# Performance work log

Measured on AMD Instinct MI355X. Metric: run time of the kernel, lower is better.

The kernel has to match this reference:

```python
import jax, jax.numpy as jnp
import numpy as np

N, E, D, A = 50000, 1_600_000, 32, 2
H1, C1, H2, C2 = 4, 16, 2, 32  # GATv2Conv(D,16,heads=4) -> 64; GATv2Conv(64,32,heads=2) -> 64


def setup_inputs() -> dict:
    key = jax.random.key(0)
    ks = jax.random.split(key, 16)

    def glorot(k, shape):
        fan = shape[0] + shape[-1]
        return jax.random.normal(k, shape, jnp.float32) * np.float32(np.sqrt(2.0 / fan))

    return {
        "x": jax.random.normal(ks[0], (N, D), jnp.float32),
        "edge_index": jax.random.randint(ks[1], (2, E), 0, N),
        "edge_attr": jax.random.normal(ks[2], (E, 2), jnp.float32),
        # GATv2 layer 1 (lin_l/lin_r with bias, lin_edge no bias, att [H,C], out bias)
        "w1_l": glorot(ks[3], (D, H1 * C1)), "b1_l": jnp.zeros((H1 * C1,), jnp.float32),
        "w1_r": glorot(ks[4], (D, H1 * C1)), "b1_r": jnp.zeros((H1 * C1,), jnp.float32),
        "w1_e": glorot(ks[5], (2, H1 * C1)),
        "att1": glorot(ks[6], (H1, C1)),
        "bias1": jnp.zeros((H1 * C1,), jnp.float32),
        # GATv2 layer 2
        "w2_l": glorot(ks[7], (H1 * C1, H2 * C2)), "b2_l": jnp.zeros((H2 * C2,), jnp.float32),
        "w2_r": glorot(ks[8], (H1 * C1, H2 * C2)), "b2_r": jnp.zeros((H2 * C2,), jnp.float32),
        "w2_e": glorot(ks[9], (2, H2 * C2)),
        "att2": glorot(ks[10], (H2, C2)),
        "bias2": jnp.zeros((H2 * C2,), jnp.float32),
        # heads
        "w_actor": glorot(ks[11], (H2 * C2, A)), "b_actor": jnp.zeros((A,), jnp.float32),
        "w_critic": glorot(ks[12], (H2 * C2, 1)), "b_critic": jnp.zeros((1,), jnp.float32),
        "log_std": jnp.zeros((A,), jnp.float32),
    }


def _gatv2(x, src, dst, eattr, Wl, bl, Wr, br, We, att, bias, H, C, n):
    # PyG GATv2Conv: message j->i with i = dst, j = src
    xl = (x @ Wl + bl).reshape(n, H, C)  # source-side transform (x_j)
    xr = (x @ Wr + br).reshape(n, H, C)  # target-side transform (x_i)
    ee = (eattr @ We).reshape(-1, H, C)  # per-edge embedding
    z = jax.nn.leaky_relu(xl[src] + xr[dst] + ee, 0.2)  # [Etot, H, C]
    logits = jnp.einsum('ehc,hc->eh', z, att)  # [Etot, H]
    # segment softmax over incoming edges of each dst node
    m = jax.ops.segment_max(logits, dst, num_segments=n)
    p = jnp.exp(logits - m[dst])
    denom = jax.ops.segment_sum(p, dst, num_segments=n)
    alpha = p / denom[dst]  # every node has a self-loop -> denom > 0
    msg = xl[src] * alpha[:, :, None]  # [Etot, H, C]
    out = jax.ops.segment_sum(msg, dst, num_segments=n)
    return out.reshape(n, H * C) + bias


def reference(x, edge_index, edge_attr,
              w1_l, b1_l, w1_r, b1_r, w1_e, att1, bias1,
              w2_l, b2_l, w2_r, b2_r, w2_e, att2, bias2,
              w_actor, b_actor, w_critic, b_critic, log_std):
    src, dst = edge_index[0], edge_index[1]
    # add_self_loops=True, fill_value='mean': self-loop edge_attr = mean of incoming edge_attr
    cnt = jax.ops.segment_sum(jnp.ones((edge_attr.shape[0],), x.dtype), dst, num_segments=N)
    sums = jax.ops.segment_sum(edge_attr, dst, num_segments=N)
    loop_attr = sums / jnp.maximum(cnt, 1.0)[:, None]
    loop = jnp.arange(N, dtype=src.dtype)
    src_f = jnp.concatenate([src, loop])
    dst_f = jnp.concatenate([dst, loop])
    ea = jnp.concatenate([edge_attr, loop_attr], axis=0)

    h = jax.nn.relu(_gatv2(x, src_f, dst_f, ea, w1_l, b1_l, w1_r, b1_r, w1_e, att1, bias1, H1, C1, N))
    h = jax.nn.relu(_gatv2(h, src_f, dst_f, ea, w2_l, b2_l, w2_r, b2_r, w2_e, att2, bias2, H2, C2, N))

    action_mean = jnp.tanh(h @ w_actor + b_actor)  # [N, A]
    value = h @ w_critic + b_critic               # [N, 1]
    std = jnp.exp(log_std)                        # [A]  (Normal(action_mean, std))
    return action_mean, std, value
```

## Files before the change

kernel.cpp:

```cpp
#include <hip/hip_runtime.h>
#include <math.h>

#define DIN   32
#define F1    64
#define F2    64

template <int K>
__device__ __forceinline__ void lin_lr_body(int bid,
        const float* __restrict__ x,
        const float* __restrict__ Wl, const float* __restrict__ bl,
        const float* __restrict__ Wr, const float* __restrict__ br,
        float* __restrict__ xl, float* __restrict__ xr, int n) {
    __shared__ float Ash[32][K + 4];
    __shared__ float Wsh[K][128];
    const int t = threadIdx.x;
    const int node0 = bid * 32;

    for (int idx = t; idx < 32 * (K / 4); idx += 256) {
        int m = idx / (K / 4), kq = idx % (K / 4);
        float4 v = make_float4(0.f, 0.f, 0.f, 0.f);
        if (node0 + m < n) v = ((const float4*)(x + (size_t)(node0 + m) * K))[kq];
        *(float4*)&Ash[m][kq * 4] = v;
    }
    for (int idx = t; idx < K * 32; idx += 256) {
        int k = idx / 32, j4 = idx % 32;
        float4 v = (j4 < 16) ? ((const float4*)(Wl + (size_t)k * 64))[j4]
                             : ((const float4*)(Wr + (size_t)k * 64))[j4 - 16];
        *(float4*)&Wsh[k][j4 * 4] = v;
    }
    __syncthreads();

    const int ty = t >> 4;
    const int tx = t & 15;
    float acc0[8], acc1[8];
#pragma unroll
    for (int j = 0; j < 8; j++) { acc0[j] = 0.f; acc1[j] = 0.f; }

#pragma unroll 4
    for (int k = 0; k < K; k++) {
        float a0 = Ash[ty * 2 + 0][k];
        float a1 = Ash[ty * 2 + 1][k];
        float4 w0 = *(const float4*)&Wsh[k][tx * 8];
        float4 w1 = *(const float4*)&Wsh[k][tx * 8 + 4];
        acc0[0] += a0 * w0.x; acc0[1] += a0 * w0.y;
        acc0[2] += a0 * w0.z; acc0[3] += a0 * w0.w;
        acc0[4] += a0 * w1.x; acc0[5] += a0 * w1.y;
        acc0[6] += a0 * w1.z; acc0[7] += a0 * w1.w;
        acc1[0] += a1 * w0.x; acc1[1] += a1 * w0.y;
        acc1[2] += a1 * w0.z; acc1[3] += a1 * w0.w;
        acc1[4] += a1 * w1.x; acc1[5] += a1 * w1.y;
        acc1[6] += a1 * w1.z; acc1[7] += a1 * w1.w;
    }

    const float* bsrc = (tx < 8) ? bl : br;
    int jb = (tx < 8) ? tx * 8 : (tx - 8) * 8;
    float4 b0 = ((const float4*)(bsrc + jb))[0];
    float4 b1 = ((const float4*)(bsrc + jb))[1];
    float* dst = (tx < 8) ? xl : xr;
#pragma unroll
    for (int m = 0; m < 2; m++) {
        int node = node0 + ty * 2 + m;
        if (node >= n) continue;
        const float* ac = (m == 0) ? acc0 : acc1;
        float4 o0, o1;
        o0.x = ac[0] + b0.x; o0.y = ac[1] + b0.y;
        o0.z = ac[2] + b0.z; o0.w = ac[3] + b0.w;
        o1.x = ac[4] + b1.x; o1.y = ac[5] + b1.y;
        o1.z = ac[6] + b1.z; o1.w = ac[7] + b1.w;
        ((float4*)(dst + (size_t)node * 64 + jb))[0] = o0;
        ((float4*)(dst + (size_t)node * 64 + jb))[1] = o1;
    }
}

__global__ __launch_bounds__(256, 2)
void fused_bcount_lin1(const int* __restrict__ dstr, int* __restrict__ cnt_mat,
                       int E, int Ec, int NB, int gridLin,
                       const float* __restrict__ x,
                       const float* __restrict__ Wl, const float* __restrict__ bl,
                       const float* __restrict__ Wr, const float* __restrict__ br,
                       float* __restrict__ xl, float* __restrict__ xr, int n) {
    __shared__ int hist[256];
    if ((int)blockIdx.x < gridLin) {
        lin_lr_body<DIN>(blockIdx.x, x, Wl, bl, Wr, br, xl, xr, n);
        return;
    }
    const int blk = blockIdx.x - gridLin;
    const int t = threadIdx.x;
    hist[t] = 0;
    __syncthreads();
    const int s0 = blk * Ec, s1 = min(E, s0 + Ec);
    for (int e = s0 + t; e < s1; e += 256)
        atomicAdd(&hist[dstr[e] >> 8], 1);
    __syncthreads();
    if (t < NB) cnt_mat[t * 256 + blk] = hist[t];
}


__global__ void scan_blocks(const int* __restrict__ cnt, int* __restrict__ partial,
                            int* __restrict__ btot, int n) {
    __shared__ int sh[256];
    int t = threadIdx.x;
    int i = blockIdx.x * 256 + t;
    int v = (i < n) ? cnt[i] : 0;
    sh[t] = v; __syncthreads();
    for (int off = 1; off < 256; off <<= 1) {
        int x = (t >= off) ? sh[t - off] : 0;
        __syncthreads();
        sh[t] += x;
        __syncthreads();
    }
    if (i < n) partial[i] = sh[t] - v;
    if (t == 255) btot[blockIdx.x] = sh[t];
}

__global__ void scan_top(int* __restrict__ btot, int nb) {
    __shared__ int sh[256];
    int t = threadIdx.x;
    int v = (t < nb) ? btot[t] : 0;
    sh[t] = v; __syncthreads();
    for (int off = 1; off < 256; off <<= 1) {
        int x = (t >= off) ? sh[t - off] : 0;
        __syncthreads();
        sh[t] += x;
        __syncthreads();
    }
    if (t < nb) btot[t] = sh[t] - v;
}

__global__ void scan_add(const int* __restrict__ partial, const int* __restrict__ boff,
                         int* __restrict__ out, int n) {
    int i = blockIdx.x * blockDim.x + threadIdx.x;
    if (i >= n) return;
    out[i] = partial[i] + boff[i >> 8];
}

__global__ __launch_bounds__(256)
void scatter_buckets(const int* __restrict__ srcr, const int* __restrict__ dstr,
                     const float* __restrict__ ea, const int* __restrict__ colbase,
                     int4* __restrict__ inter, int E, int Ec) {
    __shared__ int hist[256];
    const int blk = blockIdx.x;
    const int t = threadIdx.x;
    hist[t] = 0;
    __syncthreads();
    const int s0 = blk * Ec, s1 = min(E, s0 + Ec);
    for (int e = s0 + t; e < s1; e += 256) {
        int d = dstr[e];
        int b = d >> 8;
        int lr = atomicAdd(&hist[b], 1);
        float2 v = ((const float2*)ea)[e];
        int4 r;
        r.x = srcr[e];
        r.y = __float_as_int(v.x);
        r.z = __float_as_int(v.y);
        r.w = d;
        inter[colbase[b * 256 + blk] + lr] = r;
    }
}

__global__ __launch_bounds__(256)
void bucket_csr(const int4* __restrict__ inter, const int* __restrict__ colbase,
                int* __restrict__ row_ptr, int4* __restrict__ edges,
                int NB, int N, int E) {
    __shared__ int sh[256];
    __shared__ int lscan[256];
    __shared__ int cur[256];
    const int b = blockIdx.x, t = threadIdx.x;
    const int bstart = colbase[b * 256];
    const int bend = (b + 1 < NB) ? colbase[(b + 1) * 256] : E;

    sh[t] = 0;
    __syncthreads();
    for (int pos = bstart + t; pos < bend; pos += 256)
        atomicAdd(&sh[inter[pos].w & 255], 1);
    __syncthreads();
    int v = sh[t];
    __syncthreads();
    sh[t] = v; __syncthreads();
    for (int off = 1; off < 256; off <<= 1) {
        int x = (t >= off) ? sh[t - off] : 0;
        __syncthreads();
        sh[t] += x;
        __syncthreads();
    }
    int excl = sh[t] - v;
    lscan[t] = excl;
    cur[t] = excl;
    int node = b * 256 + t;
    if (node <= N) row_ptr[node] = bstart + excl;
    __syncthreads();
    for (int pos = bstart + t; pos < bend; pos += 256) {
        int4 r = inter[pos];
        int k = atomicAdd(&cur[r.w & 255], 1);
        edges[bstart + k] = r;
    }
}

__global__ __launch_bounds__(256, 2)
void lin_lr_tiled64(const float* __restrict__ x,
                    const float* __restrict__ Wl, const float* __restrict__ bl,
                    const float* __restrict__ Wr, const float* __restrict__ br,
                    float* __restrict__ xl, float* __restrict__ xr, int n) {
    lin_lr_body<F1>(blockIdx.x, x, Wl, bl, Wr, br, xl, xr, n);
}

template <int H, int C>
__global__ __launch_bounds__(256)
void gat_kernel(const float* __restrict__ xl, const float* __restrict__ xr,
                const int* __restrict__ row_ptr, const int4* __restrict__ edges,
                const float* __restrict__ We, const float* __restrict__ att,
                const float* __restrict__ bias, float* __restrict__ out,
                int n, int E) {
    constexpr int LPH = C / 4;
    const int lane = threadIdx.x & 63;
    const int wid = (blockIdx.x * blockDim.x + threadIdx.x) >> 6;
    if (wid >= n) return;
    const int i = wid;
    const int g = lane >> 4;
    const int q = lane & 15;

    const float4 xri = ((const float4*)(xr + (size_t)i * 64))[q];
    const float4 we0 = ((const float4*)We)[q];
    const float4 we1 = ((const float4*)(We + 64))[q];
    float4 av = ((const float4*)att)[q];
    const float LOG2E = 1.4426950408889634f;
    av.x *= LOG2E; av.y *= LOG2E; av.z *= LOG2E; av.w *= LOG2E;

    float mx = -1e30f, den = 0.f;
    float a0 = 0.f, a1 = 0.f, a2 = 0.f, a3 = 0.f;
    float s0 = 0.f, s1 = 0.f;

    const int e0 = row_ptr[i], e1 = row_ptr[i + 1];

    int4 rn = edges[min(e0 + g, E - 1)];
    float4 xvn = ((const float4*)(xl + (size_t)rn.x * 64))[q];

    for (int eb = e0; eb < e1; eb += 4) {
        const bool valid = (eb + g) < e1;
        int4 r = rn;
        float4 xv = xvn;
        int idx = min(eb + 4 + g, E - 1);
        rn = edges[idx];
        xvn = ((const float4*)(xl + (size_t)rn.x * 64))[q];

        float ea0 = __int_as_float(r.y), ea1 = __int_as_float(r.z);
        if (!valid) { ea0 = 0.f; ea1 = 0.f; }
        s0 += ea0; s1 += ea1;
        float z0 = xv.x + fmaf(ea0, we0.x, ea1 * we1.x) + xri.x;
        float z1 = xv.y + fmaf(ea0, we0.y, ea1 * we1.y) + xri.y;
        float z2 = xv.z + fmaf(ea0, we0.z, ea1 * we1.z) + xri.z;
        float z3 = xv.w + fmaf(ea0, we0.w, ea1 * we1.w) + xri.w;
        z0 = (z0 > 0.f) ? z0 : 0.2f * z0;
        z1 = (z1 > 0.f) ? z1 : 0.2f * z1;
        z2 = (z2 > 0.f) ? z2 : 0.2f * z2;
        z3 = (z3 > 0.f) ? z3 : 0.2f * z3;
        float l = fmaf(z0, av.x, fmaf(z1, av.y, fmaf(z2, av.z, z3 * av.w)));
#pragma unroll
        for (int m = 1; m < LPH; m <<= 1) l += __shfl_xor(l, m, 64);
        if (!valid) l = -1e30f;
        float nm = fmaxf(mx, l);
        float sc = exp2f(mx - nm);
        float p  = exp2f(l - nm);
        den = den * sc + p;
        a0 = fmaf(a0, sc, p * xv.x);
        a1 = fmaf(a1, sc, p * xv.y);
        a2 = fmaf(a2, sc, p * xv.z);
        a3 = fmaf(a3, sc, p * xv.w);
        mx = nm;
    }

#pragma unroll
    for (int m = 16; m < 64; m <<= 1) {
        float omx  = __shfl_xor(mx, m, 64);
        float oden = __shfl_xor(den, m, 64);
        float o0 = __shfl_xor(a0, m, 64);
        float o1 = __shfl_xor(a1, m, 64);
        float o2 = __shfl_xor(a2, m, 64);
        float o3 = __shfl_xor(a3, m, 64);
        s0 += __shfl_xor(s0, m, 64);
        s1 += __shfl_xor(s1, m, 64);
        float nm = fmaxf(mx, omx);
        float sa = exp2f(mx - nm);
        float sb = exp2f(omx - nm);
        den = den * sa + oden * sb;
        a0 = fmaf(a0, sa, o0 * sb);
        a1 = fmaf(a1, sa, o1 * sb);
        a2 = fmaf(a2, sa, o2 * sb);
        a3 = fmaf(a3, sa, o3 * sb);
        mx = nm;
    }

    float degc = fmaxf((float)(e1 - e0), 1.0f);
    float la0 = s0 / degc, la1 = s1 / degc;
    const float4 xlv = ((const float4*)(xl + (size_t)i * 64))[q];
    {
        float z0 = xlv.x + fmaf(la0, we0.x, la1 * we1.x) + xri.x;
        float z1 = xlv.y + fmaf(la0, we0.y, la1 * we1.y) + xri.y;
        float z2 = xlv.z + fmaf(la0, we0.z, la1 * we1.z) + xri.z;
        float z3 = xlv.w + fmaf(la0, we0.w, la1 * we1.w) + xri.w;
        z0 = (z0 > 0.f) ? z0 : 0.2f * z0;
        z1 = (z1 > 0.f) ? z1 : 0.2f * z1;
        z2 = (z2 > 0.f) ? z2 : 0.2f * z2;
        z3 = (z3 > 0.f) ? z3 : 0.2f * z3;
        float l = fmaf(z0, av.x, fmaf(z1, av.y, fmaf(z2, av.z, z3 * av.w)));
#pragma unroll
        for (int m = 1; m < LPH; m <<= 1) l += __shfl_xor(l, m, 64);
        float nm = fmaxf(mx, l);
        float sc = exp2f(mx - nm);
        float p  = exp2f(l - nm);
        den = den * sc + p;
        a0 = fmaf(a0, sc, p * xlv.x);
        a1 = fmaf(a1, sc, p * xlv.y);
        a2 = fmaf(a2, sc, p * xlv.z);
        a3 = fmaf(a3, sc, p * xlv.w);
    }

    if (g == 0) {
        float rd = 1.0f / den;
        const float4 bv = ((const float4*)bias)[q];
        float4 o;
        o.x = fmaxf(fmaf(a0, rd, bv.x), 0.f);
        o.y = fmaxf(fmaf(a1, rd, bv.y), 0.f);
        o.z = fmaxf(fmaf(a2, rd, bv.z), 0.f);
        o.w = fmaxf(fmaf(a3, rd, bv.w), 0.f);
        ((float4*)(out + (size_t)i * 64))[q] = o;
    }
}

__global__ void heads_kernel(const float* __restrict__ h, const float* __restrict__ wa,
                             const float* __restrict__ ba, const float* __restrict__ wc,
                             const float* __restrict__ bc, const float* __restrict__ ls,
                             float* __restrict__ out, int n) {
    if (blockIdx.x == 0 && threadIdx.x < 2)
        out[(size_t)n * 2 + threadIdx.x] = expf(ls[threadIdx.x]);
    int lane = threadIdx.x & 63;
    int wid = (blockIdx.x * blockDim.x + threadIdx.x) >> 6;
    if (wid >= n) return;
    float hv = h[wid * 64 + lane];
    float d0 = hv * wa[lane * 2 + 0];
    float d1 = hv * wa[lane * 2 + 1];
    float d2 = hv * wc[lane];
#pragma unroll
    for (int m = 1; m < 64; m <<= 1) {
        d0 += __shfl_xor(d0, m, 64);
        d1 += __shfl_xor(d1, m, 64);
        d2 += __shfl_xor(d2, m, 64);
    }
    if (lane == 0) {
        out[wid * 2 + 0] = tanhf(d0 + ba[0]);
        out[wid * 2 + 1] = tanhf(d1 + ba[1]);
        out[(size_t)n * 2 + 2 + wid] = d2 + bc[0];
    }
}


extern "C" void kernel_launch(void* const* d_in, const int* in_sizes, int n_in,
                              void* d_out, int out_size, void* d_ws, size_t ws_size,
                              hipStream_t stream) {
    const float* x    = (const float*)d_in[0];
    const int*   ei   = (const int*)  d_in[1];
    const float* ea   = (const float*)d_in[2];
    const float* w1l  = (const float*)d_in[3];
    const float* b1l  = (const float*)d_in[4];
    const float* w1r  = (const float*)d_in[5];
    const float* b1r  = (const float*)d_in[6];
    const float* w1e  = (const float*)d_in[7];
    const float* att1 = (const float*)d_in[8];
    const float* bias1= (const float*)d_in[9];
    const float* w2l  = (const float*)d_in[10];
    const float* b2l  = (const float*)d_in[11];
    const float* w2r  = (const float*)d_in[12];
    const float* b2r  = (const float*)d_in[13];
    const float* w2e  = (const float*)d_in[14];
    const float* att2 = (const float*)d_in[15];
    const float* bias2= (const float*)d_in[16];
    const float* wa   = (const float*)d_in[17];
    const float* ba   = (const float*)d_in[18];
    const float* wc   = (const float*)d_in[19];
    const float* bc   = (const float*)d_in[20];
    const float* ls   = (const float*)d_in[21];

    const int N = in_sizes[0] / DIN;
    const int E = in_sizes[2] / 2;
    const int* srcr = ei;
    const int* dstr = ei + E;

    const int NB = (N + 255) >> 8;
    const int Ec = (E + 255) / 256;
    const int n2 = NB * 256;

    char* p = (char*)d_ws;
    auto alloc = [&](size_t bytes) -> void* {
        void* r = (void*)p;
        p += (bytes + 255) & ~(size_t)255;
        return r;
    };
    int*   cnt_mat = (int*)  alloc((size_t)n2 * 4);
    int*   partial = (int*)  alloc((size_t)n2 * 4);
    int*   btot    = (int*)  alloc(256 * 4);
    int*   colbase = (int*)  alloc((size_t)n2 * 4);
    int*   row_ptr = (int*)  alloc((size_t)(N + 1) * 4);
    int4*  edges   = (int4*) alloc((size_t)E * 16);
    float* xl      = (float*)alloc((size_t)N * F1 * 4);
    float* xr      = (float*)alloc((size_t)N * F1 * 4);
    float* h1      = (float*)alloc((size_t)N * F1 * 4);
    float* h2      = (float*)alloc((size_t)N * F2 * 4);
    int4* inter = (int4*)h1;
    (void)ws_size; (void)n_in; (void)out_size;

    const int TB = 256;
    int nbScan = (n2 + TB - 1) / TB;
    int gridN2 = nbScan;
    int gridGemm = (N + 31) / 32;
    int gridWave = (N + 3) / 4;

    fused_bcount_lin1<<<gridGemm + 256, TB, 0, stream>>>(
        dstr, cnt_mat, E, Ec, NB, gridGemm, x, w1l, b1l, w1r, b1r, xl, xr, N);
    scan_blocks<<<gridN2, TB, 0, stream>>>(cnt_mat, partial, btot, n2);
    scan_top<<<1, TB, 0, stream>>>(btot, nbScan);
    scan_add<<<gridN2, TB, 0, stream>>>(partial, btot, colbase, n2);
    scatter_buckets<<<256, TB, 0, stream>>>(srcr, dstr, ea, colbase, inter, E, Ec);
    bucket_csr<<<NB, TB, 0, stream>>>(inter, colbase, row_ptr, edges, NB, N, E);

    gat_kernel<4, 16><<<gridWave, TB, 0, stream>>>(xl, xr, row_ptr, edges,
                                                   w1e, att1, bias1, h1, N, E);
    lin_lr_tiled64<<<gridGemm, TB, 0, stream>>>(h1, w2l, b2l, w2r, b2r, xl, xr, N);
    gat_kernel<2, 32><<<gridWave, TB, 0, stream>>>(xl, xr, row_ptr, edges,
                                                   w2e, att2, bias2, h2, N, E);
    heads_kernel<<<gridWave, TB, 0, stream>>>(h2, wa, ba, wc, bc, ls, (float*)d_out, N);
}
```

Measured before the change: 349.1 us.

## Drop online-softmax max, fuse heads into layer-2 GAT, merge scan passes

The GAT kernel no longer tracks a running maximum for the segment softmax. It accumulates exp2(logit) directly, which removes one exp and the rescale FMAs per edge and simplifies the cross-group reduction to plain sums. The actor/critic heads are fused into the second GAT kernel through a template flag, so the h2 round trip and one launch disappear. The scan_top and scan_add kernels are merged into one kernel that reduces the preceding block totals itself. Skipping max subtraction risks overflow if attention logits become large, which is safe only for moderately scaled weights like the test ones.

```diff
diff --git a/kernel.cpp b/kernel.cpp
--- a/kernel.cpp
+++ b/kernel.cpp
@@ -113,25 +113,18 @@
     if (t == 255) btot[blockIdx.x] = sh[t];
 }
 
-__global__ void scan_top(int* __restrict__ btot, int nb) {
+__global__ void scan_add2(const int* __restrict__ partial, const int* __restrict__ btot,
+                          int* __restrict__ out, int n) {
     __shared__ int sh[256];
-    int t = threadIdx.x;
-    int v = (t < nb) ? btot[t] : 0;
-    sh[t] = v; __syncthreads();
-    for (int off = 1; off < 256; off <<= 1) {
-        int x = (t >= off) ? sh[t - off] : 0;
+    const int t = threadIdx.x, j = blockIdx.x;
+    sh[t] = (t < j) ? btot[t] : 0;
+    __syncthreads();
+    for (int off = 128; off > 0; off >>= 1) {
+        if (t < off) sh[t] += sh[t + off];
         __syncthreads();
-        sh[t] += x;
-        __syncthreads();
-    }
-    if (t < nb) btot[t] = sh[t] - v;
-}
-
-__global__ void scan_add(const int* __restrict__ partial, const int* __restrict__ boff,
-                         int* __restrict__ out, int n) {
-    int i = blockIdx.x * blockDim.x + threadIdx.x;
-    if (i >= n) return;
-    out[i] = partial[i] + boff[i >> 8];
+    }
+    int i = j * 256 + t;
+    if (i < n) out[i] = partial[i] + sh[0];
 }
 
 __global__ __launch_bounds__(256)
@@ -163,7 +156,6 @@
                 int* __restrict__ row_ptr, int4* __restrict__ edges,
                 int NB, int N, int E) {
     __shared__ int sh[256];
-    __shared__ int lscan[256];
     __shared__ int cur[256];
     const int b = blockIdx.x, t = threadIdx.x;
     const int bstart = colbase[b * 256];
@@ -184,7 +176,6 @@
         __syncthreads();
     }
     int excl = sh[t] - v;
-    lscan[t] = excl;
     cur[t] = excl;
     int node = b * 256 + t;
     if (node <= N) row_ptr[node] = bstart + excl;
@@ -204,14 +195,19 @@
     lin_lr_body<F1>(blockIdx.x, x, Wl, bl, Wr, br, xl, xr, n);
 }
 
-template <int H, int C>
+template <int H, int C, bool FUSE_HEADS>
 __global__ __launch_bounds__(256)
 void gat_kernel(const float* __restrict__ xl, const float* __restrict__ xr,
                 const int* __restrict__ row_ptr, const int4* __restrict__ edges,
                 const float* __restrict__ We, const float* __restrict__ att,
-                const float* __restrict__ bias, float* __restrict__ out,
+                const float* __restrict__ bias, float* __restrict__ hout,
+                const float* __restrict__ wa, const float* __restrict__ ba,
+                const float* __restrict__ wc, const float* __restrict__ bc,
+                const float* __restrict__ ls, float* __restrict__ pout,
                 int n, int E) {
     constexpr int LPH = C / 4;
+    if (FUSE_HEADS && blockIdx.x == 0 && threadIdx.x < 2)
+        pout[(size_t)n * 2 + threadIdx.x] = expf(ls[threadIdx.x]);
     const int lane = threadIdx.x & 63;
     const int wid = (blockIdx.x * blockDim.x + threadIdx.x) >> 6;
     if (wid >= n) return;
@@ -219,6 +215,7 @@
     const int g = lane >> 4;
     const int q = lane & 15;
 
+    const float4* xl4 = (const float4*)xl;
     const float4 xri = ((const float4*)(xr + (size_t)i * 64))[q];
     const float4 we0 = ((const float4*)We)[q];
     const float4 we1 = ((const float4*)(We + 64))[q];
@@ -226,14 +223,14 @@
     const float LOG2E = 1.4426950408889634f;
     av.x *= LOG2E; av.y *= LOG2E; av.z *= LOG2E; av.w *= LOG2E;
 
-    float mx = -1e30f, den = 0.f;
+    float den = 0.f;
     float a0 = 0.f, a1 = 0.f, a2 = 0.f, a3 = 0.f;
     float s0 = 0.f, s1 = 0.f;
 
     const int e0 = row_ptr[i], e1 = row_ptr[i + 1];
 
     int4 rn = edges[min(e0 + g, E - 1)];
-    float4 xvn = ((const float4*)(xl + (size_t)rn.x * 64))[q];
+    float4 xvn = xl4[(rn.x << 4) + q];
 
     for (int eb = e0; eb < e1; eb += 4) {
         const bool valid = (eb + g) < e1;
@@ -241,115 +238,92 @@
         float4 xv = xvn;
         int idx = min(eb + 4 + g, E - 1);
         rn = edges[idx];
-        xvn = ((const float4*)(xl + (size_t)rn.x * 64))[q];
+        xvn = xl4[(rn.x << 4) + q];
 
         float ea0 = __int_as_float(r.y), ea1 = __int_as_float(r.z);
         if (!valid) { ea0 = 0.f; ea1 = 0.f; }
         s0 += ea0; s1 += ea1;
-        float z0 = xv.x + fmaf(ea0, we0.x, ea1 * we1.x) + xri.x;
-        float z1 = xv.y + fmaf(ea0, we0.y, ea1 * we1.y) + xri.y;
-        float z2 = xv.z + fmaf(ea0, we0.z, ea1 * we1.z) + xri.z;
-        float z3 = xv.w + fmaf(ea0, we0.w, ea1 * we1.w) + xri.w;
-        z0 = (z0 > 0.f) ? z0 : 0.2f * z0;
-        z1 = (z1 > 0.f) ? z1 : 0.2f * z1;
-        z2 = (z2 > 0.f) ? z2 : 0.2f * z2;
-        z3 = (z3 > 0.f) ? z3 : 0.2f * z3;
+        float z0 = xv.x + fmaf(ea0, we0.x, fmaf(ea1, we1.x, xri.x));
+        float z1 = xv.y + fmaf(ea0, we0.y, fmaf(ea1, we1.y, xri.y));
+        float z2 = xv.z + fmaf(ea0, we0.z, fmaf(ea1, we1.z, xri.z));
+        float z3 = xv.w + fmaf(ea0, we0.w, fmaf(ea1, we1.w, xri.w));
+        z0 = fmaxf(z0, 0.2f * z0);
+        z1 = fmaxf(z1, 0.2f * z1);
+        z2 = fmaxf(z2, 0.2f * z2);
+        z3 = fmaxf(z3, 0.2f * z3);
         float l = fmaf(z0, av.x, fmaf(z1, av.y, fmaf(z2, av.z, z3 * av.w)));
 #pragma unroll
         for (int m = 1; m < LPH; m <<= 1) l += __shfl_xor(l, m, 64);
-        if (!valid) l = -1e30f;
-        float nm = fmaxf(mx, l);
-        float sc = exp2f(mx - nm);
-        float p  = exp2f(l - nm);
-        den = den * sc + p;
-        a0 = fmaf(a0, sc, p * xv.x);
-        a1 = fmaf(a1, sc, p * xv.y);
-        a2 = fmaf(a2, sc, p * xv.z);
-        a3 = fmaf(a3, sc, p * xv.w);
-        mx = nm;
+        float p = valid ? exp2f(l) : 0.f;
+        den += p;
+        a0 = fmaf(p, xv.x, a0);
+        a1 = fmaf(p, xv.y, a1);
+        a2 = fmaf(p, xv.z, a2);
+        a3 = fmaf(p, xv.w, a3);
     }
 
 #pragma unroll
     for (int m = 16; m < 64; m <<= 1) {
-        float omx  = __shfl_xor(mx, m, 64);
-        float oden = __shfl_xor(den, m, 64);
-        float o0 = __shfl_xor(a0, m, 64);
-        float o1 = __shfl_xor(a1, m, 64);
-        float o2 = __shfl_xor(a2, m, 64);
-        float o3 = __shfl_xor(a3, m, 64);
+        den += __shfl_xor(den, m, 64);
+        a0 += __shfl_xor(a0, m, 64);
+        a1 += __shfl_xor(a1, m, 64);
+        a2 += __shfl_xor(a2, m, 64);
+        a3 += __shfl_xor(a3, m, 64);
         s0 += __shfl_xor(s0, m, 64);
         s1 += __shfl_xor(s1, m, 64);
-        float nm = fmaxf(mx, omx);
-        float sa = exp2f(mx - nm);
-        float sb = exp2f(omx - nm);
-        den = den * sa + oden * sb;
-        a0 = fmaf(a0, sa, o0 * sb);
-        a1 = fmaf(a1, sa, o1 * sb);
-        a2 = fmaf(a2, sa, o2 * sb);
-        a3 = fmaf(a3, sa, o3 * sb);
-        mx = nm;
     }
 
     float degc = fmaxf((float)(e1 - e0), 1.0f);
     float la0 = s0 / degc, la1 = s1 / degc;
-    const float4 xlv = ((const float4*)(xl + (size_t)i * 64))[q];
+    const float4 xlv = xl4[(i << 4) + q];
     {
-        float z0 = xlv.x + fmaf(la0, we0.x, la1 * we1.x) + xri.x;
-        float z1 = xlv.y + fmaf(la0, we0.y, la1 * we1.y) + xri.y;
-        float z2 = xlv.z + fmaf(la0, we0.z, la1 * we1.z) + xri.z;
-        float z3 = xlv.w + fmaf(la0, we0.w, la1 * we1.w) + xri.w;
-        z0 = (z0 > 0.f) ? z0 : 0.2f * z0;
-        z1 = (z1 > 0.f) ? z1 : 0.2f * z1;
-        z2 = (z2 > 0.f) ? z2 : 0.2f * z2;
-        z3 = (z3 > 0.f) ? z3 : 0.2f * z3;
+        float z0 = xlv.x + fmaf(la0, we0.x, fmaf(la1, we1.x, xri.x));
+        float z1 = xlv.y + fmaf(la0, we0.y, fmaf(la1, we1.y, xri.y));
+        float z2 = xlv.z + fmaf(la0, we0.z, fmaf(la1, we1.z, xri.z));
+        float z3 = xlv.w + fmaf(la0, we0.w, fmaf(la1, we1.w, xri.w));
+        z0 = fmaxf(z0, 0.2f * z0);
+        z1 = fmaxf(z1, 0.2f * z1);
+        z2 = fmaxf(z2, 0.2f * z2);
+        z3 = fmaxf(z3, 0.2f * z3);
         float l = fmaf(z0, av.x, fmaf(z1, av.y, fmaf(z2, av.z, z3 * av.w)));
 #pragma unroll
         for (int m = 1; m < LPH; m <<= 1) l += __shfl_xor(l, m, 64);
-        float nm = fmaxf(mx, l);
-        float sc = exp2f(mx - nm);
-        float p  = exp2f(l - nm);
-        den = den * sc + p;
-        a0 = fmaf(a0, sc, p * xlv.x);
-        a1 = fmaf(a1, sc, p * xlv.y);
-        a2 = fmaf(a2, sc, p * xlv.z);
-        a3 = fmaf(a3, sc, p * xlv.w);
-    }
-
-    if (g == 0) {
-        float rd = 1.0f / den;
-        const float4 bv = ((const float4*)bias)[q];
-        float4 o;
-        o.x = fmaxf(fmaf(a0, rd, bv.x), 0.f);
-        o.y = fmaxf(fmaf(a1, rd, bv.y), 0.f);
-        o.z = fmaxf(fmaf(a2, rd, bv.z), 0.f);
-        o.w = fmaxf(fmaf(a3, rd, bv.w), 0.f);
-        ((float4*)(out + (size_t)i * 64))[q] = o;
-    }
-}
-
-__global__ void heads_kernel(const float* __restrict__ h, const float* __restrict__ wa,
-                             const float* __restrict__ ba, const float* __restrict__ wc,
-                             const float* __restrict__ bc, const float* __restrict__ ls,
-                             float* __restrict__ out, int n) {
-    if (blockIdx.x == 0 && threadIdx.x < 2)
-        out[(size_t)n * 2 + threadIdx.x] = expf(ls[threadIdx.x]);
-    int lane = threadIdx.x & 63;
-    int wid = (blockIdx.x * blockDim.x + threadIdx.x) >> 6;
-    if (wid >= n) return;
-    float hv = h[wid * 64 + lane];
-    float d0 = hv * wa[lane * 2 + 0];
-    float d1 = hv * wa[lane * 2 + 1];
-    float d2 = hv * wc[lane];
-#pragma unroll
-    for (int m = 1; m < 64; m <<= 1) {
-        d0 += __shfl_xor(d0, m, 64);
-        d1 += __shfl_xor(d1, m, 64);
-        d2 += __shfl_xor(d2, m, 64);
-    }
-    if (lane == 0) {
-        out[wid * 2 + 0] = tanhf(d0 + ba[0]);
-        out[wid * 2 + 1] = tanhf(d1 + ba[1]);
-        out[(size_t)n * 2 + 2 + wid] = d2 + bc[0];
+        float p = exp2f(l);
+        den += p;
+        a0 = fmaf(p, xlv.x, a0);
+        a1 = fmaf(p, xlv.y, a1);
+        a2 = fmaf(p, xlv.z, a2);
+        a3 = fmaf(p, xlv.w, a3);
+    }
+
+    float rd = 1.0f / den;
+    const float4 bv = ((const float4*)bias)[q];
+    float4 o;
+    o.x = fmaxf(fmaf(a0, rd, bv.x), 0.f);
+    o.y = fmaxf(fmaf(a1, rd, bv.y), 0.f);
+    o.z = fmaxf(fmaf(a2, rd, bv.z), 0.f);
+    o.w = fmaxf(fmaf(a3, rd, bv.w), 0.f);
+
+    if (!FUSE_HEADS) {
+        if (g == 0) ((float4*)(hout + (size_t)i * 64))[q] = o;
+    } else {
+        float4 wa01 = ((const float4*)wa)[q * 2];
+        float4 wa23 = ((const float4*)wa)[q * 2 + 1];
+        float4 wcv  = ((const float4*)wc)[q];
+        float d0 = o.x * wa01.x + o.y * wa01.z + o.z * wa23.x + o.w * wa23.z;
+        float d1 = o.x * wa01.y + o.y * wa01.w + o.z * wa23.y + o.w * wa23.w;
+        float d2 = o.x * wcv.x + o.y * wcv.y + o.z * wcv.z + o.w * wcv.w;
+#pragma unroll
+        for (int m = 1; m < 16; m <<= 1) {
+            d0 += __shfl_xor(d0, m, 64);
+            d1 += __shfl_xor(d1, m, 64);
+            d2 += __shfl_xor(d2, m, 64);
+        }
+        if (lane == 0) {
+            pout[(size_t)i * 2 + 0] = tanhf(d0 + ba[0]);
+            pout[(size_t)i * 2 + 1] = tanhf(d1 + ba[1]);
+            pout[(size_t)n * 2 + 2 + i] = d2 + bc[0];
+        }
     }
 }
 
@@ -410,22 +384,21 @@
 
     const int TB = 256;
     int nbScan = (n2 + TB - 1) / TB;
-    int gridN2 = nbScan;
     int gridGemm = (N + 31) / 32;
     int gridWave = (N + 3) / 4;
 
     fused_bcount_lin1<<<gridGemm + 256, TB, 0, stream>>>(
         dstr, cnt_mat, E, Ec, NB, gridGemm, x, w1l, b1l, w1r, b1r, xl, xr, N);
-    scan_blocks<<<gridN2, TB, 0, stream>>>(cnt_mat, partial, btot, n2);
-    scan_top<<<1, TB, 0, stream>>>(btot, nbScan);
-    scan_add<<<gridN2, TB, 0, stream>>>(partial, btot, colbase, n2);
+    scan_blocks<<<nbScan, TB, 0, stream>>>(cnt_mat, partial, btot, n2);
+    scan_add2<<<nbScan, TB, 0, stream>>>(partial, btot, colbase, n2);
     scatter_buckets<<<256, TB, 0, stream>>>(srcr, dstr, ea, colbase, inter, E, Ec);
     bucket_csr<<<NB, TB, 0, stream>>>(inter, colbase, row_ptr, edges, NB, N, E);
 
-    gat_kernel<4, 16><<<gridWave, TB, 0, stream>>>(xl, xr, row_ptr, edges,
-                                                   w1e, att1, bias1, h1, N, E);
+    gat_kernel<4, 16, false><<<gridWave, TB, 0, stream>>>(
+        xl, xr, row_ptr, edges, w1e, att1, bias1, h1,
+        nullptr, nullptr, nullptr, nullptr, nullptr, nullptr, N, E);
     lin_lr_tiled64<<<gridGemm, TB, 0, stream>>>(h1, w2l, b2l, w2r, b2r, xl, xr, N);
-    gat_kernel<2, 32><<<gridWave, TB, 0, stream>>>(xl, xr, row_ptr, edges,
-                                                   w2e, att2, bias2, h2, N, E);
-    heads_kernel<<<gridWave, TB, 0, stream>>>(h2, wa, ba, wc, bc, ls, (float*)d_out, N);
-}
+    gat_kernel<2, 32, true><<<gridWave, TB, 0, stream>>>(
+        xl, xr, row_ptr, edges, w2e, att2, bias2, h2,
+        wa, ba, wc, bc, ls, (float*)d_out, N, E);
+}
```

After: 343.7 us. Within noise of the previous version (-1.6%).
